# Optimization experiments

Measured on AMD Instinct MI355X. Metric: run time of the kernel, lower is better.

The kernel has to match this reference:

```python
import jax, jax.numpy as jnp
import numpy as np

B, S, D_IN = 16, 1024, 1024
H, D_OUT = 16, 128

def setup_inputs() -> dict:
    key = jax.random.key(0)
    k1, k2, k3 = jax.random.split(key, 3)
    x = jax.random.normal(k1, (B, S, D_IN), dtype=jnp.float32)
    W = jax.random.normal(k2, (H, 3, D_IN, D_OUT), dtype=jnp.float32) * (1.0 / np.sqrt(D_IN))
    Wo = jax.random.normal(k3, (H * D_OUT, D_OUT), dtype=jnp.float32) * (1.0 / np.sqrt(H * D_OUT))
    return {"x": x, "W": W, "Wo": Wo}

def reference(x, W, Wo):
    # x: [B,S,D_IN], W: [H,3,D_IN,E], Wo: [H*E,E]
    E = W.shape[-1]
    q = jnp.einsum('bsd,hde->bhse', x, W[:, 0])
    k = jnp.einsum('bsd,hde->bhse', x, W[:, 1])
    v = jnp.einsum('bsd,hde->bhse', x, W[:, 2])
    # NOTE: source divides by (output_dim * 0.5), not sqrt(output_dim)
    scores = jnp.einsum('bhse,bhte->bhst', q, k) / (E * 0.5)
    attn = jax.nn.softmax(scores, axis=-1)
    o = jnp.einsum('bhst,bhte->bhse', attn, v)          # [B,H,S,E]
    o = jnp.transpose(o, (0, 2, 1, 3)).reshape(x.shape[0], x.shape[1], -1)  # concat heads
    return jnp.einsum('bsf,fe->bse', o, Wo)
```

## Files before the change

### kernel.cpp

```cpp
#include <hip/hip_runtime.h>

typedef unsigned short u16;
typedef _Float16 f16;
typedef __attribute__((ext_vector_type(8))) _Float16 half8;
typedef __attribute__((ext_vector_type(8))) short short8;
typedef __attribute__((ext_vector_type(4))) float f32x4;
typedef __attribute__((ext_vector_type(4))) float f4;
typedef __attribute__((ext_vector_type(4))) u16 u16x4;

#define B_ 16
#define S_ 1024
#define DIN_ 1024
#define H_ 16
#define E_ 128

#define EXPK 0.0225546041776533f

__device__ __forceinline__ u16 f2h(float f) {
  f16 h = (f16)f;
  return __builtin_bit_cast(u16, h);
}

__device__ __forceinline__ void gl2lds16(const u16* g, u16* l) {
  __builtin_amdgcn_global_load_lds((const __attribute__((address_space(1))) void*)g,
                                   (__attribute__((address_space(3))) void*)l, 16, 0, 0);
}

__global__ __launch_bounds__(256) void zero_f32(float* __restrict__ p) {
  int i = (blockIdx.x * 256 + threadIdx.x) * 4;
  f4 z = {0.f, 0.f, 0.f, 0.f};
  *reinterpret_cast<f4*>(p + i) = z;
}

__global__ __launch_bounds__(256) void cvt_f32_f16(const float* __restrict__ in,
                                                   u16* __restrict__ out) {
  int i = (blockIdx.x * 256 + threadIdx.x) * 4;
  f4 v = *reinterpret_cast<const f4*>(in + i);
  u16x4 o;
  o[0] = f2h(v[0]); o[1] = f2h(v[1]); o[2] = f2h(v[2]); o[3] = f2h(v[3]);
  *reinterpret_cast<u16x4*>(out + i) = o;
}

__global__ __launch_bounds__(256) void transpose_cvt(const float* __restrict__ in,
                                                     u16* __restrict__ out,
                                                     int R, int C) {
  __shared__ float tile[32][33];
  const size_t moff = (size_t)blockIdx.z * R * C;
  const float* src = in + moff;
  u16* dst = out + moff;
  int c0 = blockIdx.x * 32, r0 = blockIdx.y * 32;
  int tx = threadIdx.x & 31, ty = threadIdx.x >> 5;
#pragma unroll
  for (int i = 0; i < 32; i += 8)
    tile[ty + i][tx] = src[(size_t)(r0 + ty + i) * C + c0 + tx];
  __syncthreads();
#pragma unroll
  for (int i = 0; i < 32; i += 8)
    dst[(size_t)(c0 + ty + i) * R + r0 + tx] = f2h(tile[tx][ty + i]);
}

template<int MODE, int KSPLIT, int K>
__global__ __launch_bounds__(256) void gemm_bt(const u16* __restrict__ A,
                                               const u16* __restrict__ BT,
                                               u16* __restrict__ q, u16* __restrict__ kk,
                                               u16* __restrict__ vT, float* __restrict__ out) {
  const int tid = threadIdx.x;
  const int m0 = blockIdx.x * 128;
  const u16* Bblk = BT + (size_t)blockIdx.y * 128 * K;
  __shared__ __align__(16) u16 smem[132 * 128];
  u16* As = smem;
  u16* Bs = smem + 8192;
  const int w = tid >> 6, lane = tid & 63;
  const int quad = lane >> 4, ln = lane & 15;
  const int wr = w >> 1, wc = w & 1;

  const int kbeg = (KSPLIT > 1) ? blockIdx.z * (K / KSPLIT) : 0;
  constexpr int KLEN = K / KSPLIT;

  const int rr = lane >> 3;
  const int cc = (lane & 7) ^ rr;
  const u16* agp[4];
  const u16* bgp[4];
#pragma unroll
  for (int i = 0; i < 4; i++) {
    int row = i * 32 + w * 8 + rr;
    agp[i] = A + (size_t)(m0 + row) * K + kbeg + cc * 8;
    bgp[i] = Bblk + (size_t)row * K + kbeg + cc * 8;
  }

  int offA[4][2], offB[4][2];
#pragma unroll
  for (int mt = 0; mt < 4; mt++) {
    int row = wr * 64 + mt * 16 + ln;
#pragma unroll
    for (int k2 = 0; k2 < 2; k2++)
      offA[mt][k2] = row * 64 + (((k2 * 4 + quad) ^ (ln & 7)) * 8);
  }
#pragma unroll
  for (int nt = 0; nt < 4; nt++) {
    int row = wc * 64 + nt * 16 + ln;
#pragma unroll
    for (int k2 = 0; k2 < 2; k2++)
      offB[nt][k2] = row * 64 + (((k2 * 4 + quad) ^ (ln & 7)) * 8);
  }

  f32x4 acc[4][4];
  f32x4 zero = {0.f, 0.f, 0.f, 0.f};
#pragma unroll
  for (int mt = 0; mt < 4; mt++)
#pragma unroll
    for (int nt = 0; nt < 4; nt++) acc[mt][nt] = zero;

#pragma unroll
  for (int k0 = 0; k0 < KLEN; k0 += 64) {
    __syncthreads();
#pragma unroll
    for (int i = 0; i < 4; i++) {
      gl2lds16(agp[i] + k0, As + i * 2048 + w * 512);
      gl2lds16(bgp[i] + k0, Bs + i * 2048 + w * 512);
    }
    __syncthreads();
#pragma unroll
    for (int k2 = 0; k2 < 2; k2++) {
      half8 af[4], bfr[4];
#pragma unroll
      for (int mt = 0; mt < 4; mt++)
        af[mt] = *reinterpret_cast<const half8*>(&As[offA[mt][k2]]);
#pragma unroll
      for (int nt = 0; nt < 4; nt++)
        bfr[nt] = *reinterpret_cast<const half8*>(&Bs[offB[nt][k2]]);
#pragma unroll
      for (int mt = 0; mt < 4; mt++)
#pragma unroll
        for (int nt = 0; nt < 4; nt++)
          acc[mt][nt] = __builtin_amdgcn_mfma_f32_16x16x32_f16(af[mt], bfr[nt], acc[mt][nt], 0, 0, 0);
    }
  }

  if (MODE == 0) {
    const int h = blockIdx.y / 3, c = blockIdx.y % 3;
    if (c < 2) {
      u16* dst = (c == 0) ? q : kk;
      const float sc = (c == 0) ? EXPK : 1.0f;
#pragma unroll
      for (int mt = 0; mt < 4; mt++)
#pragma unroll
        for (int nt = 0; nt < 4; nt++)
#pragma unroll
          for (int r = 0; r < 4; r++) {
            int row = wr * 64 + mt * 16 + quad * 4 + r;
            int tok = m0 + row;
            int bb = tok >> 10, s = tok & 1023;
            int e = wc * 64 + nt * 16 + ln;
            dst[(((size_t)bb * H_ + h) * S_ + s) * E_ + e] = f2h(acc[mt][nt][r] * sc);
          }
    } else {
      __syncthreads();
#pragma unroll
      for (int mt = 0; mt < 4; mt++)
#pragma unroll
        for (int nt = 0; nt < 4; nt++)
#pragma unroll
          for (int r = 0; r < 4; r++) {
            int row = wr * 64 + mt * 16 + quad * 4 + r;
            int e = wc * 64 + nt * 16 + ln;
            int srow = (row & 64) | ((row & 15) << 2) | ((row >> 4) & 3);
            smem[e * 132 + srow] = f2h(acc[mt][nt][r]);
          }
      __syncthreads();
      const int bb = m0 >> 10, sbase = m0 & 1023;
      u16* vbase = vT + (((size_t)bb * H_ + h) * E_) * S_;
#pragma unroll
      for (int i = 0; i < 8; i++) {
        int e = (tid >> 4) + i * 16, s0 = (tid & 15) * 8;
        *reinterpret_cast<short8*>(&vbase[(size_t)e * S_ + sbase + s0]) =
            *reinterpret_cast<const short8*>(&smem[e * 132 + s0]);
      }
    }
  } else {
#pragma unroll
    for (int mt = 0; mt < 4; mt++)
#pragma unroll
      for (int nt = 0; nt < 4; nt++)
#pragma unroll
        for (int r = 0; r < 4; r++) {
          int row = wr * 64 + mt * 16 + quad * 4 + r;
          int e = wc * 64 + nt * 16 + ln;
          if (KSPLIT > 1)
            atomicAdd(&out[(size_t)(m0 + row) * E_ + e], acc[mt][nt][r]);
          else
            out[(size_t)(m0 + row) * E_ + e] = acc[mt][nt][r];
        }
  }
}

struct SmemKV {
  u16 ks[64 * 128];
  u16 vs[128 * 64];
};
union SmemAttn {
  u16 qs[128 * 132];
  SmemKV s;
};

__global__ __launch_bounds__(256, 3) void attn_kernel(const u16* __restrict__ qg,
                                                      const u16* __restrict__ kg,
                                                      const u16* __restrict__ vg,
                                                      u16* __restrict__ og) {
  __shared__ __align__(16) SmemAttn sm;
  const int tid = threadIdx.x;
  const int id = blockIdx.x;
  const int g = id >> 6, qt = (id >> 3) & 7, x = id & 7;
  const int hb = g * 8 + x;
  const int b = hb >> 4, h = hb & 15;
  const int q0 = qt * 128;
  const size_t bh = (size_t)(b * H_ + h);
  const u16* qp = qg + bh * S_ * E_;
  const u16* kp = kg + bh * S_ * E_;
  const u16* vp = vg + bh * E_ * S_;
  const int w = tid >> 6, lane = tid & 63, quad = lane >> 4, ln = lane & 15;

#pragma unroll
  for (int i = 0; i < 8; i++) {
    int idx = tid + i * 256;
    int row = idx >> 4, col = (idx & 15) * 8;
    *reinterpret_cast<short8*>(&sm.qs[row * 132 + col]) =
        *reinterpret_cast<const short8*>(&qp[(size_t)(q0 + row) * E_ + col]);
  }
  __syncthreads();
  half8 qf[2][4];
#pragma unroll
  for (int mt = 0; mt < 2; mt++)
#pragma unroll
    for (int ks = 0; ks < 4; ks++)
      qf[mt][ks] = *reinterpret_cast<const half8*>(
          &sm.qs[(w * 32 + mt * 16 + ln) * 132 + ks * 32 + quad * 8]);

  const int krow = w * 4 + (lane >> 4);
  const int kc = ((lane & 15) & 8) | (((lane & 15) & 7) ^ (krow & 7));
  const u16* kbase = kp + (size_t)krow * E_ + kc * 8;
  const int vrow = w * 8 + (lane >> 3);
  const int vc = (lane & 7) ^ ((lane >> 3) & 7);
  const u16* vbase = vp + (size_t)vrow * S_ + vc * 8;

  u16* ps = sm.s.ks;

  f32x4 zero = {0.f, 0.f, 0.f, 0.f};
  f32x4 oa[2][8];
#pragma unroll
  for (int mt = 0; mt < 2; mt++)
#pragma unroll
    for (int nt = 0; nt < 8; nt++) oa[mt][nt] = zero;
  float lsum[2][4];
#pragma unroll
  for (int mt = 0; mt < 2; mt++)
#pragma unroll
    for (int r = 0; r < 4; r++) lsum[mt][r] = 0.f;

  for (int kt = 0; kt < 16; kt++) {
    __syncthreads();
#pragma unroll
    for (int i = 0; i < 4; i++) {
      gl2lds16(kbase + (size_t)kt * 8192 + i * 16 * E_, &sm.s.ks[(i * 256 + w * 64) * 8]);
      gl2lds16(vbase + (size_t)kt * 64 + i * 32 * S_,   &sm.s.vs[(i * 256 + w * 64) * 8]);
    }
    __syncthreads();

    f32x4 sa[2][4];
#pragma unroll
    for (int mt = 0; mt < 2; mt++)
#pragma unroll
      for (int nt = 0; nt < 4; nt++) sa[mt][nt] = zero;
#pragma unroll
    for (int ks = 0; ks < 4; ks++) {
      half8 kf[4];
#pragma unroll
      for (int nt = 0; nt < 4; nt++) {
        int c = ks * 4 + quad;
        int cs = (c & 8) | ((c & 7) ^ (ln & 7));
        kf[nt] = *reinterpret_cast<const half8*>(&sm.s.ks[(nt * 16 + ln) * 128 + cs * 8]);
      }
#pragma unroll
      for (int mt = 0; mt < 2; mt++)
#pragma unroll
        for (int nt = 0; nt < 4; nt++)
          sa[mt][nt] = __builtin_amdgcn_mfma_f32_16x16x32_f16(qf[mt][ks], kf[nt], sa[mt][nt], 0, 0, 0);
    }

    u16x4 pk[2][4];
#pragma unroll
    for (int mt = 0; mt < 2; mt++) {
#pragma unroll
      for (int r = 0; r < 4; r++) {
        float psum = 0.f;
        u16x4 pp;
#pragma unroll
        for (int nt = 0; nt < 4; nt++) {
          float p = exp2f(sa[mt][nt][r]);
          psum += p;
          pp[nt] = f2h(p);
        }
        pk[mt][r] = pp;
        lsum[mt][r] += psum;
      }
    }
    __syncthreads();

#pragma unroll
    for (int mt = 0; mt < 2; mt++)
#pragma unroll
      for (int r = 0; r < 4; r++) {
        int qr = w * 32 + mt * 16 + quad * 4 + r;
        *reinterpret_cast<u16x4*>(&ps[qr * 64 + ((ln * 4) ^ ((qr & 7) << 3))]) = pk[mt][r];
      }

#pragma unroll
    for (int k2 = 0; k2 < 2; k2++) {
      half8 pf[2];
#pragma unroll
      for (int mt = 0; mt < 2; mt++)
        pf[mt] = *reinterpret_cast<const half8*>(
            &ps[(w * 32 + mt * 16 + ln) * 64 + ((k2 * 32 + quad * 8) ^ ((ln & 7) << 3))]);
#pragma unroll
      for (int nt8 = 0; nt8 < 8; nt8++) {
        int c = k2 * 4 + quad;
        int cs = c ^ (ln & 7);
        half8 vf = *reinterpret_cast<const half8*>(&sm.s.vs[(nt8 * 16 + ln) * 64 + cs * 8]);
#pragma unroll
        for (int mt = 0; mt < 2; mt++)
          oa[mt][nt8] = __builtin_amdgcn_mfma_f32_16x16x32_f16(pf[mt], vf, oa[mt][nt8], 0, 0, 0);
      }
    }
  }

#pragma unroll
  for (int mt = 0; mt < 2; mt++) {
#pragma unroll
    for (int r = 0; r < 4; r++) {
      float l = lsum[mt][r];
#pragma unroll
      for (int d = 1; d < 16; d <<= 1) l += __shfl_xor(l, d);
      float rl = 1.0f / l;
      int srow = q0 + w * 32 + mt * 16 + quad * 4 + r;
      size_t base = ((size_t)b * S_ + srow) * (H_ * E_) + (size_t)h * E_;
#pragma unroll
      for (int nt8 = 0; nt8 < 8; nt8++)
        og[base + nt8 * 16 + ln] = f2h(oa[mt][nt8][r] * rl);
    }
  }
}

extern "C" void kernel_launch(void* const* d_in, const int* in_sizes, int n_in,
                              void* d_out, int out_size, void* d_ws, size_t ws_size,
                              hipStream_t stream) {
  const float* x = (const float*)d_in[0];
  const float* W = (const float*)d_in[1];
  const float* Wo = (const float*)d_in[2];
  float* out = (float*)d_out;
  char* ws = (char*)d_ws;

  const size_t WBT_BYTES = (size_t)H_ * 3 * DIN_ * E_ * 2;
  const size_t WOT_BYTES = (size_t)H_ * E_ * E_ * 2 * 2;
  const size_t FIXED = WBT_BYTES + WOT_BYTES;

  const size_t XB_PER   = (size_t)S_ * DIN_ * 2;
  const size_t QKV_PER  = (size_t)H_ * S_ * E_ * 2;
  const size_t OB_PER   = (size_t)S_ * H_ * E_ * 2;
  const size_t PER_ITEM = XB_PER + 3 * QKV_PER + OB_PER;

  int Bc = 1;
  for (int c = 16; c >= 1; c >>= 1) {
    if (FIXED + (size_t)c * PER_ITEM <= ws_size) { Bc = c; break; }
  }

  u16* WbT = (u16*)(ws);
  u16* WoT = (u16*)(ws + WBT_BYTES);
  char* cb = ws + FIXED;
  u16* xb  = (u16*)(cb);
  u16* qb  = (u16*)(cb + (size_t)Bc * XB_PER);
  u16* kb  = (u16*)(cb + (size_t)Bc * (XB_PER + QKV_PER));
  u16* vTb = (u16*)(cb + (size_t)Bc * (XB_PER + 2 * QKV_PER));
  u16* ob  = (u16*)(cb + (size_t)Bc * (XB_PER + 3 * QKV_PER));

  zero_f32<<<out_size / 1024, 256, 0, stream>>>(out);
  transpose_cvt<<<dim3(4, 32, 48), 256, 0, stream>>>(W, WbT, DIN_, E_);
  transpose_cvt<<<dim3(4, 64, 1), 256, 0, stream>>>(Wo, WoT, H_ * E_, E_);

  for (int b0 = 0; b0 < B_; b0 += Bc) {
    const float* xc = x + (size_t)b0 * S_ * DIN_;
    cvt_f32_f16<<<Bc * S_ * DIN_ / 1024, 256, 0, stream>>>(xc, xb);
    gemm_bt<0, 1, DIN_><<<dim3(Bc * 8, 48), 256, 0, stream>>>(xb, WbT, qb, kb, vTb, nullptr);
    attn_kernel<<<Bc * 128, 256, 0, stream>>>(qb, kb, vTb, ob);
    gemm_bt<1, 4, H_ * E_><<<dim3(Bc * 8, 1, 4), 256, 0, stream>>>(ob, WoT, nullptr, nullptr,
                                                                   nullptr, out + (size_t)b0 * S_ * E_);
  }
}
```

Before: 577.0 us.

## Double-buffer K/V tiles in attention kernel with async prefetch

The attention kernel now prefetches the next K/V tile into a second LDS buffer while computing on the current one, waiting with manual vmcnt and a raw s_barrier instead of two full __syncthreads per tile. P gets its own LDS region, so it is written straight after the exp with no extra barrier, and the MFMA phases are wrapped in s_setprio. LDS use grows from about 33KB to about 80KB per block, which may lower occupancy below the 3 blocks per CU requested. The hand-written waitcnt and barrier ordering must be correct to avoid races.

```diff
diff --git a/kernel.cpp b/kernel.cpp
--- a/kernel.cpp
+++ b/kernel.cpp
@@ -194,20 +194,19 @@
   }
 }
 
-struct SmemKV {
-  u16 ks[64 * 128];
-  u16 vs[128 * 64];
-};
-union SmemAttn {
-  u16 qs[128 * 132];
-  SmemKV s;
+struct SmemAttn2 {
+  union {
+    u16 qs[128 * 132];
+    u16 kv[2][16384];
+  };
+  u16 ps[128 * 64];
 };
 
 __global__ __launch_bounds__(256, 3) void attn_kernel(const u16* __restrict__ qg,
                                                       const u16* __restrict__ kg,
                                                       const u16* __restrict__ vg,
                                                       u16* __restrict__ og) {
-  __shared__ __align__(16) SmemAttn sm;
+  __shared__ __align__(16) SmemAttn2 sm;
   const int tid = threadIdx.x;
   const int id = blockIdx.x;
   const int g = id >> 6, qt = (id >> 3) & 7, x = id & 7;
@@ -235,6 +234,7 @@
     for (int ks = 0; ks < 4; ks++)
       qf[mt][ks] = *reinterpret_cast<const half8*>(
           &sm.qs[(w * 32 + mt * 16 + ln) * 132 + ks * 32 + quad * 8]);
+  __syncthreads();
 
   const int krow = w * 4 + (lane >> 4);
   const int kc = ((lane & 15) & 8) | (((lane & 15) & 7) ^ (krow & 7));
@@ -243,8 +243,6 @@
   const int vc = (lane & 7) ^ ((lane >> 3) & 7);
   const u16* vbase = vp + (size_t)vrow * S_ + vc * 8;
 
-  u16* ps = sm.s.ks;
-
   f32x4 zero = {0.f, 0.f, 0.f, 0.f};
   f32x4 oa[2][8];
 #pragma unroll
@@ -257,20 +255,38 @@
 #pragma unroll
     for (int r = 0; r < 4; r++) lsum[mt][r] = 0.f;
 
+#pragma unroll
+  for (int i = 0; i < 4; i++) {
+    gl2lds16(kbase + i * 16 * E_, &sm.kv[0][(i * 256 + w * 64) * 8]);
+    gl2lds16(vbase + i * 32 * S_, &sm.kv[0][8192 + (i * 256 + w * 64) * 8]);
+  }
+
   for (int kt = 0; kt < 16; kt++) {
-    __syncthreads();
-#pragma unroll
-    for (int i = 0; i < 4; i++) {
-      gl2lds16(kbase + (size_t)kt * 8192 + i * 16 * E_, &sm.s.ks[(i * 256 + w * 64) * 8]);
-      gl2lds16(vbase + (size_t)kt * 64 + i * 32 * S_,   &sm.s.vs[(i * 256 + w * 64) * 8]);
-    }
-    __syncthreads();
+    const int cur = kt & 1;
+    if (kt < 15) {
+      const int nxt = cur ^ 1;
+#pragma unroll
+      for (int i = 0; i < 4; i++) {
+        gl2lds16(kbase + (size_t)(kt + 1) * 8192 + i * 16 * E_,
+                 &sm.kv[nxt][(i * 256 + w * 64) * 8]);
+        gl2lds16(vbase + (size_t)(kt + 1) * 64 + i * 32 * S_,
+                 &sm.kv[nxt][8192 + (i * 256 + w * 64) * 8]);
+      }
+      asm volatile("s_waitcnt vmcnt(8)" ::: "memory");
+    } else {
+      asm volatile("s_waitcnt vmcnt(0)" ::: "memory");
+    }
+    asm volatile("s_barrier" ::: "memory");
+
+    const u16* ksr = &sm.kv[cur][0];
+    const u16* vsr = &sm.kv[cur][8192];
 
     f32x4 sa[2][4];
 #pragma unroll
     for (int mt = 0; mt < 2; mt++)
 #pragma unroll
       for (int nt = 0; nt < 4; nt++) sa[mt][nt] = zero;
+    __builtin_amdgcn_s_setprio(1);
 #pragma unroll
     for (int ks = 0; ks < 4; ks++) {
       half8 kf[4];
@@ -278,7 +294,7 @@
       for (int nt = 0; nt < 4; nt++) {
         int c = ks * 4 + quad;
         int cs = (c & 8) | ((c & 7) ^ (ln & 7));
-        kf[nt] = *reinterpret_cast<const half8*>(&sm.s.ks[(nt * 16 + ln) * 128 + cs * 8]);
+        kf[nt] = *reinterpret_cast<const half8*>(&ksr[(nt * 16 + ln) * 128 + cs * 8]);
       }
 #pragma unroll
       for (int mt = 0; mt < 2; mt++)
@@ -286,8 +302,8 @@
         for (int nt = 0; nt < 4; nt++)
           sa[mt][nt] = __builtin_amdgcn_mfma_f32_16x16x32_f16(qf[mt][ks], kf[nt], sa[mt][nt], 0, 0, 0);
     }
-
-    u16x4 pk[2][4];
+    __builtin_amdgcn_s_setprio(0);
+
 #pragma unroll
     for (int mt = 0; mt < 2; mt++) {
 #pragma unroll
@@ -300,37 +316,33 @@
           psum += p;
           pp[nt] = f2h(p);
         }
-        pk[mt][r] = pp;
         lsum[mt][r] += psum;
+        int qr = w * 32 + mt * 16 + quad * 4 + r;
+        *reinterpret_cast<u16x4*>(&sm.ps[qr * 64 + ((ln * 4) ^ ((qr & 7) << 3))]) = pp;
       }
     }
-    __syncthreads();
-
-#pragma unroll
-    for (int mt = 0; mt < 2; mt++)
-#pragma unroll
-      for (int r = 0; r < 4; r++) {
-        int qr = w * 32 + mt * 16 + quad * 4 + r;
-        *reinterpret_cast<u16x4*>(&ps[qr * 64 + ((ln * 4) ^ ((qr & 7) << 3))]) = pk[mt][r];
-      }
-
+
+    __builtin_amdgcn_s_setprio(1);
 #pragma unroll
     for (int k2 = 0; k2 < 2; k2++) {
       half8 pf[2];
 #pragma unroll
       for (int mt = 0; mt < 2; mt++)
         pf[mt] = *reinterpret_cast<const half8*>(
-            &ps[(w * 32 + mt * 16 + ln) * 64 + ((k2 * 32 + quad * 8) ^ ((ln & 7) << 3))]);
+            &sm.ps[(w * 32 + mt * 16 + ln) * 64 + ((k2 * 32 + quad * 8) ^ ((ln & 7) << 3))]);
 #pragma unroll
       for (int nt8 = 0; nt8 < 8; nt8++) {
         int c = k2 * 4 + quad;
         int cs = c ^ (ln & 7);
-        half8 vf = *reinterpret_cast<const half8*>(&sm.s.vs[(nt8 * 16 + ln) * 64 + cs * 8]);
+        half8 vf = *reinterpret_cast<const half8*>(&vsr[(nt8 * 16 + ln) * 64 + cs * 8]);
 #pragma unroll
         for (int mt = 0; mt < 2; mt++)
           oa[mt][nt8] = __builtin_amdgcn_mfma_f32_16x16x32_f16(pf[mt], vf, oa[mt][nt8], 0, 0, 0);
       }
     }
+    __builtin_amdgcn_s_setprio(0);
+
+    asm volatile("s_barrier" ::: "memory");
   }
 
 #pragma unroll
```

New measurement: 665.7 us. 15.4% more time.
